# Kernel optimization log

Hardware: AMD Instinct MI355X
Metric: run time of the kernel (lower is better)

Reference implementation:

```python
import jax, jax.numpy as jnp
import numpy as np

RATIO = 4


def setup_inputs() -> dict:
    key = jax.random.key(0)
    ks = jax.random.split(key, 6)
    b, c, hw = 8, 64, 256
    n = (hw // RATIO) ** 2  # 4096
    return {
        "x": jax.random.normal(ks[0], (b, c, hw, hw), dtype=jnp.float32),
        "weight": jax.random.normal(ks[1], (n, n), dtype=jnp.float32) * 0.01,
        "pih_w": jax.random.normal(ks[2], (c, c, 3, 3), dtype=jnp.float32) * 0.05,
        "pih_b": jax.random.normal(ks[3], (c,), dtype=jnp.float32) * 0.05,
        "up_w": jax.random.normal(ks[4], (c, c, 4, 4), dtype=jnp.float32) * 0.05,
        "up_b": jax.random.normal(ks[5], (c,), dtype=jnp.float32) * 0.05,
    }


def reference(x, weight, pih_w, pih_b, up_w, up_b):
    b, c, h, w = x.shape
    identity = x
    # MaxPool2d(ratio)
    xp = jax.lax.reduce_window(x, -jnp.inf, jax.lax.max,
                               (1, 1, RATIO, RATIO), (1, 1, RATIO, RATIO), 'VALID')
    # 3x3 conv, pad 1
    x_pih = jax.lax.conv_general_dilated(
        xp, pih_w, window_strides=(1, 1), padding='SAME',
        dimension_numbers=('NCHW', 'OIHW', 'NCHW')) + pih_b[None, :, None, None]
    x_pih = jax.nn.relu(x_pih).reshape(b, c, -1)  # [b, c, N]
    # F.normalize(p=2, dim=2)
    nrm = jnp.sqrt(jnp.sum(x_pih * x_pih, axis=2, keepdims=True))
    nx = x_pih / jnp.maximum(nrm, 1e-12)
    # channel-channel affinity [b, c, c]
    A = jnp.einsum('bcn,bdn->bcd', nx, nx)
    # vectorized D^{-1/2}, replacing per-batch torch.diag loop
    d = 1.0 / jnp.sqrt(jnp.sum(A, axis=2) + 1e-8)  # [b, c]
    d = jnp.where(jnp.isfinite(d), d, 0.0)
    L = jnp.eye(c, dtype=x.dtype)[None] - d[:, :, None] * A * d[:, None, :]
    # diffusion: L @ x_flat @ W
    xf = xp.reshape(b, c, -1)  # [b, c, N]
    out = jnp.einsum('bcd,bdn->bcn', L, xf)
    out = jnp.einsum('bcn,nm->bcm', out, weight)
    hp, wp = h // RATIO, w // RATIO
    out = out.reshape(b, c, hp, wp)
    # ConvTranspose2d(k=4, s=4): each pixel expands to a 4x4 block
    up = jnp.einsum('bchw,coij->bohiwj', out, up_w).reshape(b, c, h, w)
    up = up + up_b[None, :, None, None]
    return jax.nn.relu(up + identity)
```

## Files before the change

kernel.cpp:

```cpp
#include <hip/hip_runtime.h>

#define NB 8
#define NC 64
#define HW 256
#define HP 64
#define NN 4096

typedef unsigned short u16;
typedef unsigned int u32;
typedef __attribute__((ext_vector_type(8))) short s16x8;
typedef __attribute__((ext_vector_type(8))) unsigned short u16x8;
typedef __attribute__((ext_vector_type(4))) float f32x4;

__device__ __forceinline__ u16 f2bf(float f) {
    unsigned u = __float_as_uint(f);
    return (u16)((u + 0x7fffu + ((u >> 16) & 1u)) >> 16);
}
__device__ __forceinline__ float bf2f(u16 v) {
    return __uint_as_float(((unsigned)v) << 16);
}

#define GLOAD16(gsrc, ldst) \
    __builtin_amdgcn_global_load_lds((const __attribute__((address_space(1))) unsigned int*)(gsrc), \
                                     (__attribute__((address_space(3))) unsigned int*)(ldst), 16, 0, 0)

__global__ __launch_bounds__(256) void maxpool_nhwc_k(const float* __restrict__ x,
                                                      u16* __restrict__ xpc) {
    __shared__ u16 tile[64 * 66];
    int bid = blockIdx.x;
    int b = bid >> 6, y = bid & 63;
    int t = threadIdx.x;
    int cl  = t >> 3;
    int seg = t & 7;
#pragma unroll
    for (int pass = 0; pass < 2; ++pass) {
        int c = pass * 32 + cl;
        const float* p = x + ((long)(b * 64 + c) * 256 + y * 4) * 256 + seg * 32;
        float m[8];
#pragma unroll
        for (int i = 0; i < 8; ++i) m[i] = -3.4e38f;
#pragma unroll
        for (int r = 0; r < 4; ++r)
#pragma unroll
            for (int i = 0; i < 8; ++i) {
                float4 v = *(const float4*)(p + r * 256 + i * 4);
                m[i] = fmaxf(m[i], fmaxf(fmaxf(v.x, v.y), fmaxf(v.z, v.w)));
            }
#pragma unroll
        for (int i = 0; i < 8; ++i) tile[c * 66 + seg * 8 + i] = f2bf(m[i]);
    }
    __syncthreads();
    int xo = t >> 2, cp = t & 3;
    u16x8 o0, o1;
#pragma unroll
    for (int e = 0; e < 8; ++e) o0[e] = tile[(cp * 16 + e) * 66 + xo];
#pragma unroll
    for (int e = 0; e < 8; ++e) o1[e] = tile[(cp * 16 + 8 + e) * 66 + xo];
    u16* dst = xpc + ((long)(b * 4096 + y * 64 + xo)) * 64 + cp * 16;
    *(u16x8*)dst = o0;
    *(u16x8*)(dst + 8) = o1;
}

__global__ __launch_bounds__(256) void transWb_k(const float* __restrict__ W,
                                                 u16* __restrict__ WTb) {
    __shared__ float tile[64 * 65];
    int k0 = blockIdx.x * 64;
    int n0 = blockIdx.y * 64;
    int t = threadIdx.x;
#pragma unroll
    for (int i = 0; i < 4; ++i) {
        int idx = t + i * 256;
        int r  = idx >> 4;
        int c4 = (idx & 15) * 4;
        float4 v = *(const float4*)&W[(long)(k0 + r) * 4096 + n0 + c4];
        tile[(c4 + 0) * 65 + r] = v.x;
        tile[(c4 + 1) * 65 + r] = v.y;
        tile[(c4 + 2) * 65 + r] = v.z;
        tile[(c4 + 3) * 65 + r] = v.w;
    }
    __syncthreads();
#pragma unroll
    for (int i = 0; i < 2; ++i) {
        int chunk = t + i * 256;
        int nr = chunk >> 3;
        int kc = (chunk & 7) * 8;
        u16x8 o;
#pragma unroll
        for (int j = 0; j < 8; ++j) o[j] = f2bf(tile[nr * 65 + kc + j]);
        *(u16x8*)&WTb[(long)(n0 + nr) * 4096 + k0 + kc] = o;
    }
}

__global__ __launch_bounds__(256) void prep_k(const float* __restrict__ uw,
                                              const float* __restrict__ pw,
                                              u16* __restrict__ Wb,
                                              u16* __restrict__ Bpack) {
    int bid = blockIdx.x;
    int t = threadIdx.x;
    if (bid < 256) {
        int idx = bid * 256 + t;
        int c = idx & 63;
        int n = idx >> 6;
        int o = n >> 4, i = (n >> 2) & 3, j = n & 3;
        Wb[idx] = f2bf(uw[((c * 64 + o) * 4 + i) * 4 + j]);
    } else {
        int idx = (bid - 256) * 256 + t;
        if (idx >= 36864) return;
        int e = idx & 7, l = (idx >> 3) & 63, nf = (idx >> 9) & 3, s = idx >> 11;
        int ch = s & 1, kd = s >> 1;
        int dy = kd / 3, dx = kd % 3;
        int o  = nf * 16 + (l & 15);
        int ci = ch * 32 + (l >> 4) * 8 + e;
        Bpack[idx] = f2bf(pw[((o * 64 + ci) * 3 + dy) * 3 + dx]);
    }
}

__global__ __launch_bounds__(256) void conv_mfma_k(const u16* __restrict__ xpc,
                                                   const u16* __restrict__ Bpack,
                                                   const float* __restrict__ pb,
                                                   u16* __restrict__ xpihb) {
    __shared__ alignas(16) u16 ldsIn[3 * 66 * 64];
    int bid = blockIdx.x;
    int b = bid >> 6, y = bid & 63;
    int t = threadIdx.x;
    int w = t >> 6, l = t & 63;
    int lr = l & 15, ksub = l >> 4;

    if (t < 48) {
        int r = t >> 4, q = t & 15;
        int off = r * 8448 + (q < 8 ? q * 16 : 8320 + (q - 8) * 16);
        *(u16x8*)((char*)ldsIn + off) = (u16x8){0, 0, 0, 0, 0, 0, 0, 0};
    }
#pragma unroll
    for (int i = 0; i < 6; ++i) {
        int r  = i >> 1;
        int ya = y - 1 + r;
        int wro = (i & 1) * 4096 + t * 16;
        int dst = r * 8448 + 128 + wro;
        if (ya >= 0 && ya < 64) {
            int xsl = 1 + (wro >> 7);
            int srcoff = (wro & ~127) | ((wro & 127) ^ ((xsl & 7) << 4));
            GLOAD16((const char*)xpc + (long)(b * 64 + ya) * 8192 + srcoff,
                    (char*)ldsIn + dst);
        } else {
            *(u16x8*)((char*)ldsIn + dst) = (u16x8){0, 0, 0, 0, 0, 0, 0, 0};
        }
    }
    __syncthreads();

    f32x4 acc[4];
#pragma unroll
    for (int mf = 0; mf < 4; ++mf) acc[mf] = (f32x4){0.f, 0.f, 0.f, 0.f};

#pragma unroll
    for (int kd = 0; kd < 9; ++kd) {
        int dy = kd / 3, dx = kd % 3;
#pragma unroll
        for (int ch = 0; ch < 2; ++ch) {
            int s = kd * 2 + ch;
            s16x8 bfrag = *(const s16x8*)(Bpack + ((s * 4 + w) * 64 + l) * 8);
#pragma unroll
            for (int mf = 0; mf < 4; ++mf) {
                int xsl  = mf * 16 + lr + dx;
                int coff = (ch * 64 + ksub * 16) ^ ((xsl & 7) << 4);
                s16x8 af = *(const s16x8*)((const char*)ldsIn +
                                           dy * 8448 + xsl * 128 + coff);
                acc[mf] = __builtin_amdgcn_mfma_f32_16x16x32_bf16(
                    af, bfrag, acc[mf], 0, 0, 0);
            }
        }
    }
    int o = w * 16 + lr;
    float bias = pb[o];
    u16* dst = xpihb + ((long)(b * 64 + o)) * 4096 + y * 64;
#pragma unroll
    for (int mf = 0; mf < 4; ++mf)
#pragma unroll
        for (int rp = 0; rp < 2; ++rp) {
            u16 lo = f2bf(fmaxf(acc[mf][rp * 2]     + bias, 0.f));
            u16 hi = f2bf(fmaxf(acc[mf][rp * 2 + 1] + bias, 0.f));
            *(u32*)&dst[mf * 16 + ksub * 4 + rp * 2] = (u32)lo | ((u32)hi << 16);
        }
}

__global__ __launch_bounds__(256) void gram_mfma_k(const u16* __restrict__ xpihb,
                                                   float* __restrict__ G) {
    __shared__ alignas(16) u16 lds[64 * 128];
    int n0 = blockIdx.x * 128;
    int b  = blockIdx.y;
    int t = threadIdx.x;
    int w = t >> 6, l = t & 63;
    int lr = l & 15, ksub = l >> 4;
#pragma unroll
    for (int i = 0; i < 4; ++i) {
        int d = i * 4096 + t * 16;
        int row = d >> 8, off = d & 255;
        GLOAD16((const char*)xpihb + ((long)(b * 64 + row)) * 8192 + n0 * 2 +
                (off ^ ((row & 15) << 4)),
                (char*)lds + d);
    }
    __syncthreads();

    f32x4 acc[4];
#pragma unroll
    for (int mf = 0; mf < 4; ++mf) acc[mf] = (f32x4){0.f, 0.f, 0.f, 0.f};
#pragma unroll
    for (int kk = 0; kk < 4; ++kk) {
        int brow = w * 16 + lr;
        s16x8 bf = *(const s16x8*)((const char*)lds + brow * 256 +
                                   ((kk * 64 + ksub * 16) ^ ((brow & 15) << 4)));
#pragma unroll
        for (int mf = 0; mf < 4; ++mf) {
            int arow = mf * 16 + lr;
            s16x8 af = *(const s16x8*)((const char*)lds + arow * 256 +
                                       ((kk * 64 + ksub * 16) ^ ((arow & 15) << 4)));
            acc[mf] = __builtin_amdgcn_mfma_f32_16x16x32_bf16(af, bf, acc[mf], 0, 0, 0);
        }
    }
    float* Gb = G + b * 4096;
#pragma unroll
    for (int mf = 0; mf < 4; ++mf)
#pragma unroll
        for (int r = 0; r < 4; ++r)
            atomicAdd(&Gb[(mf * 16 + (l >> 4) * 4 + r) * 64 + w * 16 + lr],
                      acc[mf][r]);
}

__global__ __launch_bounds__(256) void diffuse_mfma_k(const float* __restrict__ G,
                                                      const u16* __restrict__ xpc,
                                                      u16* __restrict__ Ab16) {
    __shared__ alignas(16) u16 lds[128 * 64];
    __shared__ alignas(16) u16 ldsL[64 * 64];
    __shared__ float nrm[64], dvv[64];
    int n0 = blockIdx.x * 128;
    int b  = blockIdx.y;
    int t = threadIdx.x;
    int w = t >> 6, l = t & 63;
    int lr = l & 15, ksub = l >> 4;

#pragma unroll
    for (int i = 0; i < 4; ++i) {
        int d = i * 4096 + t * 16;
        int row = d >> 7, off = d & 127;
        GLOAD16((const char*)xpc + ((long)(b * 4096 + n0 + row)) * 128 +
                (off ^ ((row & 7) << 4)),
                (char*)lds + d);
    }

    const float* Gb = G + b * 4096;
    if (t < 64) nrm[t] = fmaxf(sqrtf(Gb[t * 64 + t]), 1e-12f);
    __syncthreads();
    if (t < 64) {
        float nc = nrm[t];
        float rs = 0.f;
        for (int d = 0; d < 64; ++d) rs += Gb[t * 64 + d] / (nc * nrm[d]);
        float dd = 1.0f / sqrtf(rs + 1e-8f);
        if (!(dd <= 3.0e38f)) dd = 0.0f;
        dvv[t] = dd;
    }
    __syncthreads();
    {
        int c = t >> 2;
        int dbase = (t & 3) * 16;
        float nc = nrm[c], dc = dvv[c];
#pragma unroll
        for (int dp2 = 0; dp2 < 8; ++dp2) {
            int d0 = dbase + dp2 * 2;
            float A0 = Gb[c * 64 + d0]     / (nc * nrm[d0]);
            float A1 = Gb[c * 64 + d0 + 1] / (nc * nrm[d0 + 1]);
            float v0 = ((c == d0)     ? 1.f : 0.f) - dc * A0 * dvv[d0];
            float v1 = ((c == d0 + 1) ? 1.f : 0.f) - dc * A1 * dvv[d0 + 1];
            int o = c * 64 + (d0 ^ ((c & 7) << 3));
            *(u32*)&ldsL[o] = (u32)f2bf(v0) | ((u32)f2bf(v1) << 16);
        }
    }
    __syncthreads();

    f32x4 acc[4][2];
#pragma unroll
    for (int mf = 0; mf < 4; ++mf)
#pragma unroll
        for (int nq = 0; nq < 2; ++nq) acc[mf][nq] = (f32x4){0.f, 0.f, 0.f, 0.f};

#pragma unroll
    for (int kk = 0; kk < 2; ++kk) {
        s16x8 bfr[2];
#pragma unroll
        for (int nq = 0; nq < 2; ++nq) {
            int brow = w * 32 + nq * 16 + lr;
            bfr[nq] = *(const s16x8*)((const char*)lds + brow * 128 +
                                      ((kk * 64 + ksub * 16) ^ ((brow & 7) << 4)));
        }
#pragma unroll
        for (int mf = 0; mf < 4; ++mf) {
            int arow = mf * 16 + lr;
            s16x8 af = *(const s16x8*)((const char*)ldsL + arow * 128 +
                                       ((kk * 64 + ksub * 16) ^ ((arow & 7) << 4)));
#pragma unroll
            for (int nq = 0; nq < 2; ++nq)
                acc[mf][nq] = __builtin_amdgcn_mfma_f32_16x16x32_bf16(
                    af, bfr[nq], acc[mf][nq], 0, 0, 0);
        }
    }
#pragma unroll
    for (int mf = 0; mf < 4; ++mf)
#pragma unroll
        for (int nq = 0; nq < 2; ++nq)
#pragma unroll
            for (int r = 0; r < 4; ++r)
                Ab16[((long)(b * 64 + mf * 16 + (l >> 4) * 4 + r)) * 4096 +
                     n0 + w * 32 + nq * 16 + lr] = f2bf(acc[mf][nq][r]);
}

#define KSPLIT 4
#define KSLICE 1024
__global__ __launch_bounds__(256) void gemm_mfma_k(const u16* __restrict__ A,
                                                   const u16* __restrict__ WT,
                                                   u16* __restrict__ Cp) {
    __shared__ alignas(16) u16 ldsA[2][8192];
    __shared__ alignas(16) u16 ldsB[2][8192];
    int bid = blockIdx.x;
    int swz = (bid & 7) * 64 + (bid >> 3);
    int m0 = (swz & 3) * 128;
    int n0 = ((swz >> 2) & 31) * 128;
    int z  = swz >> 7;
    int t = threadIdx.x;
    int w = t >> 6, l = t & 63;
    int wr = w >> 1, wc = w & 1;
    int lr = l & 15;
    int lk = (l >> 4) << 4;

    f32x4 acc[4][4];
#pragma unroll
    for (int mf = 0; mf < 4; ++mf)
#pragma unroll
        for (int nf = 0; nf < 4; ++nf) acc[mf][nf] = (f32x4){0.f, 0.f, 0.f, 0.f};

    const char* Ab = (const char*)(A  + (long)m0 * 4096 + z * KSLICE);
    const char* Bb = (const char*)(WT + (long)n0 * 4096 + z * KSLICE);

    auto stage = [&](int buf, int k0) {
#pragma unroll
        for (int i = 0; i < 4; ++i) {
            int d   = i * 4096 + t * 16;
            int row = d >> 7;
            int off = d & 127;
            int sk  = off ^ ((row & 7) << 4);
            GLOAD16(Ab + (long)row * 8192 + k0 * 2 + sk, (char*)ldsA[buf] + d);
            GLOAD16(Bb + (long)row * 8192 + k0 * 2 + sk, (char*)ldsB[buf] + d);
        }
    };

    stage(0, 0);
    __syncthreads();
    int cur = 0;
    for (int k0 = 0; k0 < KSLICE; k0 += 64) {
        if (k0 + 64 < KSLICE) stage(cur ^ 1, k0 + 64);
#pragma unroll
        for (int kk = 0; kk < 2; ++kk) {
            s16x8 af[4], bf[4];
#pragma unroll
            for (int f = 0; f < 4; ++f) {
                int ar = wr * 64 + f * 16 + lr;
                af[f] = *(const s16x8*)((const char*)ldsA[cur] + ar * 128 +
                                        ((kk * 64 + lk) ^ ((ar & 7) << 4)));
                int br = wc * 64 + f * 16 + lr;
                bf[f] = *(const s16x8*)((const char*)ldsB[cur] + br * 128 +
                                        ((kk * 64 + lk) ^ ((br & 7) << 4)));
            }
#pragma unroll
            for (int mf = 0; mf < 4; ++mf)
#pragma unroll
                for (int nf = 0; nf < 4; ++nf)
                    acc[mf][nf] = __builtin_amdgcn_mfma_f32_16x16x32_bf16(
                        af[mf], bf[nf], acc[mf][nf], 0, 0, 0);
        }
        __syncthreads();
        cur ^= 1;
    }
    int tile = (swz & 3) * 32 + ((swz >> 2) & 31);
    u16 carr[64];
#pragma unroll
    for (int mf = 0; mf < 4; ++mf)
#pragma unroll
        for (int nf = 0; nf < 4; ++nf)
#pragma unroll
            for (int r = 0; r < 4; ++r)
                carr[mf * 16 + nf * 4 + r] = f2bf(acc[mf][nf][r]);
    u16* dp = Cp + ((long)(z * 128 + tile) * 256 + t) * 64;
#pragma unroll
    for (int v8 = 0; v8 < 8; ++v8)
        *(u16x8*)&dp[v8 * 8] = *(const u16x8*)&carr[v8 * 8];
}

__global__ __launch_bounds__(256) void reduce4T_k(const u16* __restrict__ Cp,
                                                  u16* __restrict__ A2) {
    __shared__ u16 ldsT[128 * 128];
    int tile = blockIdx.x;
    int tm = tile >> 5, tn = tile & 31;
    int n0 = tn * 128;
    int t = threadIdx.x;
    int w = t >> 6, l = t & 63;
    int wr = w >> 1, wc = w & 1, lr = l & 15;

    float s[64];
#pragma unroll
    for (int k = 0; k < 64; ++k) s[k] = 0.f;

    const u16* dp = Cp + ((long)tile * 256 + t) * 64;
#pragma unroll
    for (int z = 0; z < KSPLIT; ++z) {
        const u16* pz = dp + (long)z * 128 * 256 * 64;
#pragma unroll
        for (int v8 = 0; v8 < 8; ++v8) {
            u16x8 vv = *(const u16x8*)&pz[v8 * 8];
#pragma unroll
            for (int e = 0; e < 8; ++e) s[v8 * 8 + e] += bf2f(vv[e]);
        }
    }
#pragma unroll
    for (int mf = 0; mf < 4; ++mf)
#pragma unroll
        for (int nf = 0; nf < 4; ++nf) {
            int mbase = wr * 64 + mf * 16 + (l >> 4) * 4;
            int pix   = wc * 64 + nf * 16 + lr;
            int g = (mbase >> 3) ^ (pix & 7);
            int o = pix * 128 + g * 8 + (mbase & 7);
            u32 w0 = (u32)f2bf(s[mf * 16 + nf * 4 + 0]) |
                     ((u32)f2bf(s[mf * 16 + nf * 4 + 1]) << 16);
            u32 w1 = (u32)f2bf(s[mf * 16 + nf * 4 + 2]) |
                     ((u32)f2bf(s[mf * 16 + nf * 4 + 3]) << 16);
            *(u32*)&ldsT[o]     = w0;
            *(u32*)&ldsT[o + 2] = w1;
        }
    __syncthreads();
    int pix_l = t >> 1, bh = t & 1;
    u16* dst = A2 + ((long)((2 * tm + bh) * 4096 + n0 + pix_l)) * 64;
#pragma unroll
    for (int gg = 0; gg < 8; ++gg) {
        int q = bh * 8 + gg;
        u16x8 vv = *(const u16x8*)&ldsT[pix_l * 128 + (q ^ (pix_l & 7)) * 8];
        *(u16x8*)&dst[gg * 8] = vv;
    }
}

__global__ __launch_bounds__(256) void convT_mfma_k(const u16* __restrict__ A2,
                                                    const u16* __restrict__ Wb,
                                                    const float* __restrict__ ub,
                                                    const float* __restrict__ x,
                                                    float* __restrict__ out) {
    __shared__ alignas(16) char smem[34816];
    u16*   ldsA = (u16*)smem;
    u16*   ldsB = (u16*)(smem + 16384);
    float* ldsC = (float*)smem;
    int mt = blockIdx.x;
    int nt = blockIdx.y;
    int m0 = mt * 128;
    int n0 = nt * 128;
    int t = threadIdx.x;
    int w = t >> 6, l = t & 63;
    int wr = w >> 1, wc = w & 1;
    int lr = l & 15;
    int lkb = (l >> 4) << 4;

    const char* Ab = (const char*)(A2 + (long)m0 * 64);
    const char* Bb = (const char*)(Wb + (long)n0 * 64);
#pragma unroll
    for (int i = 0; i < 4; ++i) {
        int d = i * 4096 + t * 16;
        int srcoff = (d & ~127) | ((d & 127) ^ (((d >> 7) & 7) << 4));
        GLOAD16(Ab + srcoff, (char*)ldsA + d);
        GLOAD16(Bb + srcoff, (char*)ldsB + d);
    }
    __syncthreads();

    f32x4 acc[4][4];
#pragma unroll
    for (int mf = 0; mf < 4; ++mf)
#pragma unroll
        for (int nf = 0; nf < 4; ++nf) acc[mf][nf] = (f32x4){0.f, 0.f, 0.f, 0.f};

#pragma unroll
    for (int kk = 0; kk < 2; ++kk) {
        s16x8 af[4], bfg[4];
#pragma unroll
        for (int f = 0; f < 4; ++f) {
            int ar = wr * 64 + f * 16 + lr;
            af[f] = *(const s16x8*)((const char*)ldsA + ar * 128 +
                                    ((kk * 64 + lkb) ^ ((ar & 7) << 4)));
            int br = wc * 64 + f * 16 + lr;
            bfg[f] = *(const s16x8*)((const char*)ldsB + br * 128 +
                                     ((kk * 64 + lkb) ^ ((br & 7) << 4)));
        }
#pragma unroll
        for (int mf = 0; mf < 4; ++mf)
#pragma unroll
            for (int nf = 0; nf < 4; ++nf)
                acc[mf][nf] = __builtin_amdgcn_mfma_f32_16x16x32_bf16(
                    af[mf], bfg[nf], acc[mf][nf], 0, 0, 0);
    }
    __syncthreads();

#pragma unroll
    for (int nh = 0; nh < 2; ++nh) {
        if (nh) __syncthreads();
        if (wc == nh) {
#pragma unroll
            for (int mf = 0; mf < 4; ++mf)
#pragma unroll
                for (int nf = 0; nf < 4; ++nf)
#pragma unroll
                    for (int r = 0; r < 4; ++r) {
                        int row = wr * 64 + mf * 16 + (l >> 4) * 4 + r;
                        int col = nf * 16 + lr;
                        ldsC[row * 68 + (col ^ (((row >> 3) & 7) << 2))] =
                            acc[mf][nf][r];
                    }
        }
        __syncthreads();
#pragma unroll
        for (int q = 0; q < 2; ++q) {
            int idx = q * 256 + t;
            int ml = idx & 127;
            int oo = idx >> 7;
            int o  = nt * 8 + nh * 4 + oo;
            float bias = ub[o];
            int mg = m0 + ml;
            int b = mg >> 12, pix = mg & 4095;
            int h = pix >> 6, ww = pix & 63;
            long base = ((long)(b * 64 + o) * 256 + h * 4) * 256 + ww * 4;
#pragma unroll
            for (int i = 0; i < 4; ++i) {
                f32x4 cv = *(const f32x4*)&ldsC[ml * 68 +
                            ((oo * 16 + i * 4) ^ (((ml >> 3) & 7) << 2))];
                float4 xi = *(const float4*)&x[base + i * 256];
                float4 rr;
                rr.x = fmaxf(cv[0] + bias + xi.x, 0.f);
                rr.y = fmaxf(cv[1] + bias + xi.y, 0.f);
                rr.z = fmaxf(cv[2] + bias + xi.z, 0.f);
                rr.w = fmaxf(cv[3] + bias + xi.w, 0.f);
                *(float4*)&out[base + i * 256] = rr;
            }
        }
    }
}

extern "C" void kernel_launch(void* const* d_in, const int* in_sizes, int n_in,
                              void* d_out, int out_size, void* d_ws, size_t ws_size,
                              hipStream_t stream) {
    const float* x      = (const float*)d_in[0];
    const float* weight = (const float*)d_in[1];
    const float* pih_w  = (const float*)d_in[2];
    const float* pih_b  = (const float*)d_in[3];
    const float* up_w   = (const float*)d_in[4];
    const float* up_b   = (const float*)d_in[5];
    float* out = (float*)d_out;
    float* ws  = (float*)d_ws;

    u16*   xpc   = (u16*)ws;
    u16*   xpihb = (u16*)(ws + 2097152);
    u16*   Ab16  = (u16*)(ws + 3145728);
    float* G     = ws + 4194304;
    u16*   Wb    = (u16*)(ws + 4259840);
    u16*   WTb   = (u16*)(ws + 4325376);
    u16*   Cp    = (u16*)(ws + 12713984);
    u16*   Bpack = Cp + 2097152;
    u16*   A2    = (u16*)ws;

    hipMemsetAsync(G, 0, 32768 * sizeof(float), stream);
    maxpool_nhwc_k<<<512, 256, 0, stream>>>(x, xpc);
    transWb_k     <<<dim3(64, 64), 256, 0, stream>>>(weight, WTb);
    prep_k        <<<400, 256, 0, stream>>>(up_w, pih_w, Wb, Bpack);
    conv_mfma_k   <<<512, 256, 0, stream>>>(xpc, Bpack, pih_b, xpihb);
    gram_mfma_k   <<<dim3(32, 8), 256, 0, stream>>>(xpihb, G);
    diffuse_mfma_k<<<dim3(32, 8), 256, 0, stream>>>(G, xpc, Ab16);
    gemm_mfma_k   <<<512, 256, 0, stream>>>(Ab16, WTb, Cp);
    reduce4T_k    <<<128, 256, 0, stream>>>(Cp, A2);
    convT_mfma_k  <<<dim3(256, 8), 256, 0, stream>>>(A2, Wb, up_b, x, out);
}
```

Baseline: 182.4 us.

## Fuse conv with Gram computation and single-buffer the diffusion GEMM

The 3x3 conv kernel now writes its relu'd bf16 output tile into shared memory and immediately computes the partial channel Gram matrix from it, atomically adding into G. This removes the xpihb global buffer and the separate gram kernel launch. Separately, the main GEMM drops its double-buffered LDS staging for a single buffer with a sync before and after each load, which halves its LDS use but removes the overlap of loads with MFMA work. The fused conv also issues more atomics, since each of its 512 blocks now adds a 64x64 partial into G where the old gram kernel used 256 blocks.

```diff
diff --git a/kernel.cpp b/kernel.cpp
--- a/kernel.cpp
+++ b/kernel.cpp
@@ -115,11 +115,12 @@
     }
 }
 
-__global__ __launch_bounds__(256) void conv_mfma_k(const u16* __restrict__ xpc,
-                                                   const u16* __restrict__ Bpack,
-                                                   const float* __restrict__ pb,
-                                                   u16* __restrict__ xpihb) {
+__global__ __launch_bounds__(256) void convgram_k(const u16* __restrict__ xpc,
+                                                  const u16* __restrict__ Bpack,
+                                                  const float* __restrict__ pb,
+                                                  float* __restrict__ G) {
     __shared__ alignas(16) u16 ldsIn[3 * 66 * 64];
+    __shared__ alignas(16) u16 ldsX[64 * 64];
     int bid = blockIdx.x;
     int b = bid >> 6, y = bid & 63;
     int t = threadIdx.x;
@@ -172,58 +173,41 @@
     }
     int o = w * 16 + lr;
     float bias = pb[o];
-    u16* dst = xpihb + ((long)(b * 64 + o)) * 4096 + y * 64;
 #pragma unroll
     for (int mf = 0; mf < 4; ++mf)
 #pragma unroll
         for (int rp = 0; rp < 2; ++rp) {
             u16 lo = f2bf(fmaxf(acc[mf][rp * 2]     + bias, 0.f));
             u16 hi = f2bf(fmaxf(acc[mf][rp * 2 + 1] + bias, 0.f));
-            *(u32*)&dst[mf * 16 + ksub * 4 + rp * 2] = (u32)lo | ((u32)hi << 16);
-        }
-}
-
-__global__ __launch_bounds__(256) void gram_mfma_k(const u16* __restrict__ xpihb,
-                                                   float* __restrict__ G) {
-    __shared__ alignas(16) u16 lds[64 * 128];
-    int n0 = blockIdx.x * 128;
-    int b  = blockIdx.y;
-    int t = threadIdx.x;
-    int w = t >> 6, l = t & 63;
-    int lr = l & 15, ksub = l >> 4;
-#pragma unroll
-    for (int i = 0; i < 4; ++i) {
-        int d = i * 4096 + t * 16;
-        int row = d >> 8, off = d & 255;
-        GLOAD16((const char*)xpihb + ((long)(b * 64 + row)) * 8192 + n0 * 2 +
-                (off ^ ((row & 15) << 4)),
-                (char*)lds + d);
-    }
-    __syncthreads();
-
-    f32x4 acc[4];
-#pragma unroll
-    for (int mf = 0; mf < 4; ++mf) acc[mf] = (f32x4){0.f, 0.f, 0.f, 0.f};
-#pragma unroll
-    for (int kk = 0; kk < 4; ++kk) {
-        int brow = w * 16 + lr;
-        s16x8 bf = *(const s16x8*)((const char*)lds + brow * 256 +
-                                   ((kk * 64 + ksub * 16) ^ ((brow & 15) << 4)));
-#pragma unroll
-        for (int mf = 0; mf < 4; ++mf) {
-            int arow = mf * 16 + lr;
-            s16x8 af = *(const s16x8*)((const char*)lds + arow * 256 +
-                                       ((kk * 64 + ksub * 16) ^ ((arow & 15) << 4)));
-            acc[mf] = __builtin_amdgcn_mfma_f32_16x16x32_bf16(af, bf, acc[mf], 0, 0, 0);
+            int nb   = (mf * 16 + ksub * 4 + rp * 2) * 2;
+            int boff = nb ^ ((o & 7) << 4);
+            *(u32*)((char*)ldsX + o * 128 + boff) = (u32)lo | ((u32)hi << 16);
+        }
+    __syncthreads();
+
+    f32x4 g[4];
+#pragma unroll
+    for (int nf = 0; nf < 4; ++nf) g[nf] = (f32x4){0.f, 0.f, 0.f, 0.f};
+#pragma unroll
+    for (int kk = 0; kk < 2; ++kk) {
+        int kb = kk * 64 + ksub * 16;
+        int arow = w * 16 + lr;
+        s16x8 af = *(const s16x8*)((const char*)ldsX + arow * 128 +
+                                   (kb ^ ((arow & 7) << 4)));
+#pragma unroll
+        for (int nf = 0; nf < 4; ++nf) {
+            int brow = nf * 16 + lr;
+            s16x8 bf = *(const s16x8*)((const char*)ldsX + brow * 128 +
+                                       (kb ^ ((brow & 7) << 4)));
+            g[nf] = __builtin_amdgcn_mfma_f32_16x16x32_bf16(af, bf, g[nf], 0, 0, 0);
         }
     }
     float* Gb = G + b * 4096;
 #pragma unroll
-    for (int mf = 0; mf < 4; ++mf)
+    for (int nf = 0; nf < 4; ++nf)
 #pragma unroll
         for (int r = 0; r < 4; ++r)
-            atomicAdd(&Gb[(mf * 16 + (l >> 4) * 4 + r) * 64 + w * 16 + lr],
-                      acc[mf][r]);
+            atomicAdd(&Gb[(w * 16 + ksub * 4 + r) * 64 + nf * 16 + lr], g[nf][r]);
 }
 
 __global__ __launch_bounds__(256) void diffuse_mfma_k(const float* __restrict__ G,
@@ -317,8 +301,8 @@
 __global__ __launch_bounds__(256) void gemm_mfma_k(const u16* __restrict__ A,
                                                    const u16* __restrict__ WT,
                                                    u16* __restrict__ Cp) {
-    __shared__ alignas(16) u16 ldsA[2][8192];
-    __shared__ alignas(16) u16 ldsB[2][8192];
+    __shared__ alignas(16) u16 ldsA[8192];
+    __shared__ alignas(16) u16 ldsB[8192];
     int bid = blockIdx.x;
     int swz = (bid & 7) * 64 + (bid >> 3);
     int m0 = (swz & 3) * 128;
@@ -339,33 +323,28 @@
     const char* Ab = (const char*)(A  + (long)m0 * 4096 + z * KSLICE);
     const char* Bb = (const char*)(WT + (long)n0 * 4096 + z * KSLICE);
 
-    auto stage = [&](int buf, int k0) {
+    for (int k0 = 0; k0 < KSLICE; k0 += 64) {
+        __syncthreads();
 #pragma unroll
         for (int i = 0; i < 4; ++i) {
             int d   = i * 4096 + t * 16;
             int row = d >> 7;
             int off = d & 127;
             int sk  = off ^ ((row & 7) << 4);
-            GLOAD16(Ab + (long)row * 8192 + k0 * 2 + sk, (char*)ldsA[buf] + d);
-            GLOAD16(Bb + (long)row * 8192 + k0 * 2 + sk, (char*)ldsB[buf] + d);
-        }
-    };
-
-    stage(0, 0);
-    __syncthreads();
-    int cur = 0;
-    for (int k0 = 0; k0 < KSLICE; k0 += 64) {
-        if (k0 + 64 < KSLICE) stage(cur ^ 1, k0 + 64);
+            GLOAD16(Ab + (long)row * 8192 + k0 * 2 + sk, (char*)ldsA + d);
+            GLOAD16(Bb + (long)row * 8192 + k0 * 2 + sk, (char*)ldsB + d);
+        }
+        __syncthreads();
 #pragma unroll
         for (int kk = 0; kk < 2; ++kk) {
             s16x8 af[4], bf[4];
 #pragma unroll
             for (int f = 0; f < 4; ++f) {
                 int ar = wr * 64 + f * 16 + lr;
-                af[f] = *(const s16x8*)((const char*)ldsA[cur] + ar * 128 +
+                af[f] = *(const s16x8*)((const char*)ldsA + ar * 128 +
                                         ((kk * 64 + lk) ^ ((ar & 7) << 4)));
                 int br = wc * 64 + f * 16 + lr;
-                bf[f] = *(const s16x8*)((const char*)ldsB[cur] + br * 128 +
+                bf[f] = *(const s16x8*)((const char*)ldsB + br * 128 +
                                         ((kk * 64 + lk) ^ ((br & 7) << 4)));
             }
 #pragma unroll
@@ -375,8 +354,6 @@
                     acc[mf][nf] = __builtin_amdgcn_mfma_f32_16x16x32_bf16(
                         af[mf], bf[nf], acc[mf][nf], 0, 0, 0);
         }
-        __syncthreads();
-        cur ^= 1;
     }
     int tile = (swz & 3) * 32 + ((swz >> 2) & 31);
     u16 carr[64];
@@ -558,7 +535,6 @@
     float* ws  = (float*)d_ws;
 
     u16*   xpc   = (u16*)ws;
-    u16*   xpihb = (u16*)(ws + 2097152);
     u16*   Ab16  = (u16*)(ws + 3145728);
     float* G     = ws + 4194304;
     u16*   Wb    = (u16*)(ws + 4259840);
@@ -571,8 +547,7 @@
     maxpool_nhwc_k<<<512, 256, 0, stream>>>(x, xpc);
     transWb_k     <<<dim3(64, 64), 256, 0, stream>>>(weight, WTb);
     prep_k        <<<400, 256, 0, stream>>>(up_w, pih_w, Wb, Bpack);
-    conv_mfma_k   <<<512, 256, 0, stream>>>(xpc, Bpack, pih_b, xpihb);
-    gram_mfma_k   <<<dim3(32, 8), 256, 0, stream>>>(xpihb, G);
+    convgram_k    <<<512, 256, 0, stream>>>(xpc, Bpack, pih_b, G);
     diffuse_mfma_k<<<dim3(32, 8), 256, 0, stream>>>(G, xpc, Ab16);
     gemm_mfma_k   <<<512, 256, 0, stream>>>(Ab16, WTb, Cp);
     reduce4T_k    <<<128, 256, 0, stream>>>(Cp, A2);
```

Result: faster. 168.0 us (-7.9%).
